# Optimization experiments

Hardware: AMD Instinct MI355X
Metric: run time of the kernel (lower is better)

The kernel has to match this reference:

```python
import jax, jax.numpy as jnp
import numpy as np

# Module hyperparameters (defaults from OrdinalPeakedCELoss.__init__)
K = 9
ALPHA = 0.4
W_FAR = 7.0
DELTA_FAR = 0.15
W_TAIL = 9.0
TAIL_POWER = 3
W_LPEAK = 12.0
PROB_MARGIN = 0.35
W_EMD = 1.2
CE_WEIGHT = 1.0
EPS = 1e-8
INV_LOGK = float(1.0 / np.log(K))
WIDTHS = np.array([3, 7, 10, 10, 10, 10, 10, 10, 25], dtype=np.float32)


def setup_inputs() -> dict:
    key = jax.random.key(0)
    k1, k2 = jax.random.split(key)
    B = 4_194_304
    logits = jax.random.normal(k1, (B, K), dtype=jnp.float32)
    y = jax.random.randint(k2, (B,), 0, K, dtype=jnp.int32)
    return {"logits": logits, "y": y}


def _loss(logits, y):
    # constant tables (tiny, [K,K])
    classes = jnp.arange(K, dtype=logits.dtype)
    d_idx = jnp.abs(classes[None, :] - classes[:, None])           # [K,K]
    tail_weights = jnp.where(d_idx > 1, (d_idx - 1.0) ** TAIL_POWER, 0.0)
    widths = jnp.asarray(WIDTHS, dtype=logits.dtype)
    cdf_weights = widths / widths.sum()                            # [K]

    # CE (class_weights are all ones -> plain NLL mean), normalized by log K
    logp = jax.nn.log_softmax(logits, axis=1)                      # [B,K]
    nll = -jnp.take_along_axis(logp, y[:, None], axis=1)[:, 0]     # [B]
    ce_loss = nll.mean() * INV_LOGK * CE_WEIGHT

    # probs: softmax, clamp_min(eps), renormalize
    probs = jax.nn.softmax(logits, axis=1)
    probs = jnp.maximum(probs, EPS)
    probs = probs / probs.sum(axis=1, keepdims=True)               # [B,K]

    py = jnp.take_along_axis(probs, y[:, None], axis=1)[:, 0]      # [B]

    # FarProbMargin: max prob among classes with |k-y|>1
    far_mask = d_idx[y] > 1                                        # [B,K]
    far_vals = jnp.where(far_mask, probs, -jnp.inf)
    far_max = jnp.max(far_vals, axis=1)
    far_max = jnp.where(jnp.isfinite(far_max), far_max, 0.0)
    far_margin = jax.nn.relu(far_max - (py - DELTA_FAR)).mean()

    # TailWeighted
    tail = (probs * tail_weights[y]).sum(axis=1).mean()            # [B] -> scalar

    # LocalPeak: neighbors y-1 / y+1 (0 when out of range)
    yl = jnp.clip(y - 1, 0, K - 1)
    yr = jnp.clip(y + 1, 0, K - 1)
    py_left = jnp.where(y > 0, jnp.take_along_axis(probs, yl[:, None], axis=1)[:, 0], 0.0)
    py_right = jnp.where(y + 1 < K, jnp.take_along_axis(probs, yr[:, None], axis=1)[:, 0], 0.0)
    neighbor_max = jnp.maximum(py_left, py_right)
    local_peak = jax.nn.relu(neighbor_max - (py - PROB_MARGIN)).mean()

    # EMD^2 over weighted CDFs
    cdf_pred = jnp.cumsum(probs, axis=1)                           # [B,K]
    cdf_true = (jnp.arange(K)[None, :] <= y[:, None]).astype(probs.dtype)
    emd2 = (((cdf_pred - cdf_true) ** 2) * cdf_weights).sum(axis=1).mean()

    ord_block = W_FAR * far_margin + W_TAIL * tail + W_LPEAK * local_peak + W_EMD * emd2
    return ce_loss + ALPHA * ord_block


def reference(logits, y):
    return _loss(logits, y)
```

## Files before the change

kernel.cpp:

```cpp
#include <hip/hip_runtime.h>
#include <math.h>

#define KC 9
#define BLOCK 256
#define NBLOCKS 1024
#define ROWS_TILE 1024
#define TILE_DWORDS (ROWS_TILE * KC)
#define TILE_F4 (TILE_DWORDS / 4)
#define F4_PER_THREAD (TILE_F4 / BLOCK)
#define ROWS_PER_THREAD (ROWS_TILE / BLOCK)

__device__ __forceinline__ float row_loss(const float x[KC], int yv) {
    constexpr float ALPHA = 0.4f;
    constexpr float W_FAR = 7.0f;
    constexpr float DELTA_FAR = 0.15f;
    constexpr float W_TAIL = 9.0f;
    constexpr float W_LPEAK = 12.0f;
    constexpr float PROB_MARGIN = 0.35f;
    constexpr float INV_LOGK = 0.45511961331341866f;
    constexpr float w[KC] = {3.0f/105.0f, 7.0f/105.0f, 10.0f/105.0f, 10.0f/105.0f,
                             10.0f/105.0f, 10.0f/105.0f, 10.0f/105.0f, 10.0f/105.0f,
                             25.0f/105.0f};

    float e[KC];
    float s = 0.0f;
    #pragma unroll
    for (int k = 0; k < KC; ++k) { e[k] = __expf(x[k]); s += e[k]; }
    const float inv_s = __frcp_rn(s);

    float xy = 0.0f;
    #pragma unroll
    for (int k = 0; k < KC; ++k) xy = (k == yv) ? x[k] : xy;
    const float nll = __logf(s) - xy;

    float p[KC];
    #pragma unroll
    for (int k = 0; k < KC; ++k) p[k] = e[k] * inv_s;

    float py = 0.0f, pl = 0.0f, pr = 0.0f, far_max = 0.0f, tail = 0.0f;
    float cdf = 0.0f, emd = 0.0f;
    #pragma unroll
    for (int k = 0; k < KC; ++k) {
        const int d = k - yv;
        const int ad = (d < 0) ? -d : d;
        py = (d == 0) ? p[k] : py;
        pl = (d == -1) ? p[k] : pl;
        pr = (d == 1) ? p[k] : pr;
        if (ad > 1) {
            far_max = fmaxf(far_max, p[k]);
            const float dm = (float)(ad - 1);
            tail = fmaf(p[k], dm * dm * dm, tail);
        }
        cdf += p[k];
        const float tt = (k <= yv) ? 1.0f : 0.0f;
        const float dlt = cdf - tt;
        emd = fmaf(dlt * dlt, w[k], emd);
    }

    const float far_margin = fmaxf(far_max - (py - DELTA_FAR), 0.0f);
    const float local_peak = fmaxf(fmaxf(pl, pr) - (py - PROB_MARGIN), 0.0f);

    return nll * INV_LOGK +
           ALPHA * (W_FAR * far_margin + W_TAIL * tail +
                    W_LPEAK * local_peak + 1.2f * emd);
}

__global__ __launch_bounds__(BLOCK) void ordinal_loss_kernel(
    const float* __restrict__ logits, const int* __restrict__ y,
    float* __restrict__ partials, int B, float invB)
{
    __shared__ float tile[TILE_DWORDS];
    __shared__ float wave_sums[BLOCK / 64];

    const int t = threadIdx.x;
    float acc = 0.0f;

    const int numTiles = B / ROWS_TILE;
    for (int tl = blockIdx.x; tl < numTiles; tl += NBLOCKS) {
        const float4* __restrict__ src =
            reinterpret_cast<const float4*>(logits) + (size_t)tl * TILE_F4;
        float4* dst = reinterpret_cast<float4*>(tile);
        #pragma unroll
        for (int j = 0; j < F4_PER_THREAD; ++j)
            dst[t + j * BLOCK] = src[t + j * BLOCK];
        __syncthreads();

        const int ybase = tl * ROWS_TILE;
        #pragma unroll
        for (int rr = 0; rr < ROWS_PER_THREAD; ++rr) {
            const int lr = t + rr * BLOCK;
            const int yv = y[ybase + lr];
            float x[KC];
            #pragma unroll
            for (int k = 0; k < KC; ++k) x[k] = tile[lr * KC + k];
            acc += row_loss(x, yv);
        }
        __syncthreads();
    }

    for (int r = numTiles * ROWS_TILE + blockIdx.x * BLOCK + t; r < B;
         r += NBLOCKS * BLOCK) {
        const float* row = logits + (size_t)r * KC;
        float x[KC];
        #pragma unroll
        for (int k = 0; k < KC; ++k) x[k] = row[k];
        acc += row_loss(x, y[r]);
    }

    float v = acc;
    #pragma unroll
    for (int off = 32; off > 0; off >>= 1) v += __shfl_down(v, off, 64);
    if ((t & 63) == 0) wave_sums[t >> 6] = v;
    __syncthreads();
    if (t == 0) {
        float bs = 0.0f;
        #pragma unroll
        for (int wv = 0; wv < BLOCK / 64; ++wv) bs += wave_sums[wv];
        partials[blockIdx.x] = bs * invB;
    }
}

__global__ __launch_bounds__(BLOCK) void reduce_kernel(
    const float* __restrict__ partials, float* __restrict__ out)
{
    __shared__ float wave_sums[BLOCK / 64];
    const int t = threadIdx.x;
    float v = 0.0f;
    #pragma unroll
    for (int j = 0; j < NBLOCKS / BLOCK; ++j) v += partials[t + j * BLOCK];
    #pragma unroll
    for (int off = 32; off > 0; off >>= 1) v += __shfl_down(v, off, 64);
    if ((t & 63) == 0) wave_sums[t >> 6] = v;
    __syncthreads();
    if (t == 0) out[0] = wave_sums[0] + wave_sums[1] + wave_sums[2] + wave_sums[3];
}

extern "C" void kernel_launch(void* const* d_in, const int* in_sizes, int n_in,
                              void* d_out, int out_size, void* d_ws, size_t ws_size,
                              hipStream_t stream) {
    const float* logits = (const float*)d_in[0];
    const int* y = (const int*)d_in[1];
    float* out = (float*)d_out;
    float* partials = (float*)d_ws;
    const int B = in_sizes[1];

    hipLaunchKernelGGL(ordinal_loss_kernel, dim3(NBLOCKS), dim3(BLOCK), 0, stream,
                       logits, y, partials, B, 1.0f / (float)B);
    hipLaunchKernelGGL(reduce_kernel, dim3(1), dim3(BLOCK), 0, stream,
                       partials, out);
}
```

Baseline: 226.3 us.

## Load four rows per thread directly with float4 instead of LDS tiling

Replaces the shared-memory tile staging with per-thread vector loads of four consecutive rows (nine float4s) plus an int4 of labels, removing the LDS round-trip and both block barriers per tile. The grid also doubles to 2048 blocks. The cost is strided per-lane global accesses that are less coalesced than the old cooperative copy, and higher register pressure from holding 36 logits per thread.

```diff
diff --git a/kernel.cpp b/kernel.cpp
--- a/kernel.cpp
+++ b/kernel.cpp
@@ -3,14 +3,10 @@
 
 #define KC 9
 #define BLOCK 256
-#define NBLOCKS 1024
-#define ROWS_TILE 1024
-#define TILE_DWORDS (ROWS_TILE * KC)
-#define TILE_F4 (TILE_DWORDS / 4)
-#define F4_PER_THREAD (TILE_F4 / BLOCK)
-#define ROWS_PER_THREAD (ROWS_TILE / BLOCK)
+#define NBLOCKS 2048
+#define RPC 4
 
-__device__ __forceinline__ float row_loss(const float x[KC], int yv) {
+__device__ __forceinline__ float row_loss(const float* __restrict__ x, int yv) {
     constexpr float ALPHA = 0.4f;
     constexpr float W_FAR = 7.0f;
     constexpr float DELTA_FAR = 0.15f;
@@ -69,37 +65,33 @@
     const float* __restrict__ logits, const int* __restrict__ y,
     float* __restrict__ partials, int B, float invB)
 {
-    __shared__ float tile[TILE_DWORDS];
     __shared__ float wave_sums[BLOCK / 64];
 
     const int t = threadIdx.x;
+    const int tid = blockIdx.x * BLOCK + t;
+    const int total = NBLOCKS * BLOCK;
+    const int numChunks = B / RPC;
+
     float acc = 0.0f;
 
-    const int numTiles = B / ROWS_TILE;
-    for (int tl = blockIdx.x; tl < numTiles; tl += NBLOCKS) {
+    for (int c = tid; c < numChunks; c += total) {
         const float4* __restrict__ src =
-            reinterpret_cast<const float4*>(logits) + (size_t)tl * TILE_F4;
-        float4* dst = reinterpret_cast<float4*>(tile);
+            reinterpret_cast<const float4*>(logits) + (size_t)c * 9;
+        float xall[RPC * KC];
         #pragma unroll
-        for (int j = 0; j < F4_PER_THREAD; ++j)
-            dst[t + j * BLOCK] = src[t + j * BLOCK];
-        __syncthreads();
-
-        const int ybase = tl * ROWS_TILE;
-        #pragma unroll
-        for (int rr = 0; rr < ROWS_PER_THREAD; ++rr) {
-            const int lr = t + rr * BLOCK;
-            const int yv = y[ybase + lr];
-            float x[KC];
-            #pragma unroll
-            for (int k = 0; k < KC; ++k) x[k] = tile[lr * KC + k];
-            acc += row_loss(x, yv);
+        for (int j = 0; j < 9; ++j) {
+            const float4 q = src[j];
+            xall[4*j+0] = q.x; xall[4*j+1] = q.y;
+            xall[4*j+2] = q.z; xall[4*j+3] = q.w;
         }
-        __syncthreads();
+        const int4 y4 = *(reinterpret_cast<const int4*>(y) + c);
+        acc += row_loss(&xall[0],      y4.x);
+        acc += row_loss(&xall[KC],     y4.y);
+        acc += row_loss(&xall[2*KC],   y4.z);
+        acc += row_loss(&xall[3*KC],   y4.w);
     }
 
-    for (int r = numTiles * ROWS_TILE + blockIdx.x * BLOCK + t; r < B;
-         r += NBLOCKS * BLOCK) {
+    for (int r = numChunks * RPC + tid; r < B; r += total) {
         const float* row = logits + (size_t)r * KC;
         float x[KC];
         #pragma unroll
```

New measurement: 225.4 us. About the same (-0.4%).
